# Kernel optimization log

Measured on AMD Instinct MI355X. Metric: run time of the kernel, lower is better.

The kernel has to match this reference:

```python
import jax, jax.numpy as jnp
import numpy as np

B, T, D_IN, D_H, D_OUT = 32, 2048, 1024, 1024, 1024

def setup_inputs() -> dict:
    key = jax.random.key(0)
    k1, k2, k3, k4, k5 = jax.random.split(key, 5)
    s = jax.random.normal(k1, (B, D_IN), dtype=jnp.float32)
    h = jax.random.normal(k2, (B, T, D_H), dtype=jnp.float32)
    # params (original uses np.random.random, i.e. uniform [0,1); scale kept modest)
    W_a = jax.random.uniform(k3, (D_IN, D_OUT), dtype=jnp.float32)
    U_a = jax.random.uniform(k4, (D_H, D_OUT), dtype=jnp.float32)
    v_a = jax.random.uniform(k5, (D_OUT,), dtype=jnp.float32)
    return {"s": s, "h": h, "W_a": W_a, "U_a": U_a, "v_a": v_a}

def reference(s, h, W_a, U_a, v_a):
    # Bahdanau additive attention:
    # e_bt = v_a . tanh(s W_a + h_t U_a);  a = softmax_t(e);  c_b = sum_t a_bt h_bt
    u_a_h = jnp.einsum('bth,ho->bto', h, U_a)            # [B,T,O]
    w_a_s = jnp.einsum('bi,io->bo', s, W_a)[:, None, :]  # [B,1,O]
    e = jnp.einsum('bto,o->bt', jnp.tanh(w_a_s + u_a_h), v_a)  # [B,T]
    a = jax.nn.softmax(e, axis=-1)                       # [B,T]
    c = jnp.einsum('bt,bth->bh', a, h)                   # [B,H]
    return c
```

## Files before the change

### kernel.cpp

```cpp
#include <hip/hip_runtime.h>
#include <hip/hip_bf16.h>
#include <stdint.h>

#define Bb 32
#define Tt 2048
#define Dd 1024

typedef float    f32x4 __attribute__((ext_vector_type(4)));
typedef _Float16 f16x8 __attribute__((ext_vector_type(8)));
typedef uint32_t u32;

#define WS_E     131072
#define WS_A     393216
#define WS_CP    655360
#define WS_UT    4849664

__device__ __forceinline__ void gll16(const void* g, const void* lds) {
  __builtin_amdgcn_global_load_lds(
      (const __attribute__((address_space(1))) u32*)(uintptr_t)g,
      (__attribute__((address_space(3))) u32*)(uint32_t)(uintptr_t)lds,
      16, 0, 0);
}

__global__ __launch_bounds__(256) void k_ws(const float* __restrict__ s,
                                            const float* __restrict__ W,
                                            float* __restrict__ w2_ws) {
  const int b = blockIdx.x >> 2;
  const int o = (blockIdx.x & 3) * 256 + threadIdx.x;
  __shared__ float s_sh[Dd];
#pragma unroll
  for (int j = 0; j < 4; ++j)
    s_sh[threadIdx.x + 256 * j] = s[b * Dd + threadIdx.x + 256 * j];
  __syncthreads();
  float acc = 0.f;
#pragma unroll 8
  for (int i = 0; i < Dd; ++i) acc += s_sh[i] * W[(size_t)i * Dd + o];
  w2_ws[b * Dd + o] = 2.f * acc;
}

__global__ __launch_bounds__(256) void k_ut(const float* __restrict__ U,
                                            uint8_t* __restrict__ U_ts) {
  const int i0 = (blockIdx.x >> 4) * 64;
  const int o0 = (blockIdx.x & 15) * 64;
  __shared__ float tile[64][65];
  const int tx = threadIdx.x & 63;
  const int ty = threadIdx.x >> 6;
#pragma unroll
  for (int jj = 0; jj < 16; ++jj)
    tile[tx][ty + 4 * jj] = U[(size_t)(i0 + ty + 4 * jj) * Dd + o0 + tx];
  __syncthreads();
#pragma unroll
  for (int it = 0; it < 2; ++it) {
    const int g = it * 256 + threadIdx.x;
    const int o_loc = g & 63;
    const int kg = g >> 6;
    const int o = o0 + o_loc;
    const int k = i0 + kg * 8;
    f16x8 r;
#pragma unroll
    for (int m = 0; m < 8; ++m) r[m] = (_Float16)tile[o_loc][kg * 8 + m];
    const int c    = (o >> 5) * 4 + (k >> 8);
    const int kk   = (k >> 5) & 7;
    const int half = (o >> 4) & 1;
    const int ln   = ((k >> 3) & 3) * 16 + (o & 15);
    *(f16x8*)(U_ts + (size_t)c * 16384 + kk * 2048 + half * 1024 + ln * 16) = r;
  }
}

__global__ __launch_bounds__(256, 2) void k_e(const float* __restrict__ h,
                                              const uint8_t* __restrict__ U_ts,
                                              const float* __restrict__ w2_ws,
                                              const float* __restrict__ v_a,
                                              float* __restrict__ e_ws) {
  const int b    = blockIdx.x >> 5;
  const int t0   = (blockIdx.x & 31) << 6;
  const int lane = threadIdx.x & 63;
  const int wv   = threadIdx.x >> 6;
  const int kh   = wv & 1;
  const int th   = wv >> 1;

  __shared__ __align__(16) uint8_t ubuf[2][16384];
  __shared__ __align__(16) float   exch[2048];

  f16x8 hreg[32];
  {
    const int tcol = t0 + th * 32 + (lane & 15);
    const int kgrp = (lane >> 4) * 8;
    const float* hb0 = h + ((size_t)b * Tt + tcol) * Dd;
    const float* hb1 = hb0 + (size_t)16 * Dd;
#pragma unroll
    for (int ss = 0; ss < 16; ++ss) {
      const int kbase = (ss >> 2) * 256 + kh * 128 + (ss & 3) * 32 + kgrp;
      f32x4 p0 = *(const f32x4*)(hb0 + kbase);
      f32x4 p1 = *(const f32x4*)(hb0 + kbase + 4);
      f16x8 r;
      r[0] = (_Float16)p0[0]; r[1] = (_Float16)p0[1];
      r[2] = (_Float16)p0[2]; r[3] = (_Float16)p0[3];
      r[4] = (_Float16)p1[0]; r[5] = (_Float16)p1[1];
      r[6] = (_Float16)p1[2]; r[7] = (_Float16)p1[3];
      hreg[ss * 2] = r;
      p0 = *(const f32x4*)(hb1 + kbase);
      p1 = *(const f32x4*)(hb1 + kbase + 4);
      r[0] = (_Float16)p0[0]; r[1] = (_Float16)p0[1];
      r[2] = (_Float16)p0[2]; r[3] = (_Float16)p0[3];
      r[4] = (_Float16)p1[0]; r[5] = (_Float16)p1[1];
      r[6] = (_Float16)p1[2]; r[7] = (_Float16)p1[3];
      hreg[ss * 2 + 1] = r;
    }
  }

  auto stage = [&](int c, int buf) {
    const uint8_t* src = U_ts + (size_t)c * 16384 + (size_t)(wv * 4) * 1024 + (size_t)lane * 16;
#pragma unroll
    for (int q = 0; q < 4; ++q)
      gll16(src + q * 1024, &ubuf[buf][(wv * 4 + q) * 1024]);
  };

  stage(0, 0);
  __syncthreads();

  float ep0 = 0.f, ep1 = 0.f;
  const float* wp  = w2_ws + b * Dd;
  const int    obl = kh * 16 + ((lane >> 4) << 2);

  for (int ot = 0; ot < 32; ++ot) {
    const f32x4 w4 = *(const f32x4*)(wp + (ot << 5) + obl);
    const f32x4 v4 = *(const f32x4*)(v_a + (ot << 5) + obl);
    f32x4 accA0 = {0.f,0.f,0.f,0.f}, accA1 = {0.f,0.f,0.f,0.f};
    f32x4 accB0 = {0.f,0.f,0.f,0.f}, accB1 = {0.f,0.f,0.f,0.f};
#pragma unroll
    for (int kc = 0; kc < 4; ++kc) {
      const int c   = ot * 4 + kc;
      const int cur = kc & 1;
      if (c + 1 < 128) stage(c + 1, cur ^ 1);
      const uint8_t* ub = &ubuf[cur][0] + kh * 8192 + lane * 16;
#pragma unroll
      for (int kkl = 0; kkl < 4; ++kkl) {
        const f16x8 a0 = *(const f16x8*)(ub + kkl * 2048);
        const f16x8 a1 = *(const f16x8*)(ub + kkl * 2048 + 1024);
        const f16x8 b0 = hreg[(kc * 4 + kkl) * 2];
        const f16x8 b1 = hreg[(kc * 4 + kkl) * 2 + 1];
        accA0 = __builtin_amdgcn_mfma_f32_16x16x32_f16(a0, b0, accA0, 0, 0, 0);
        accA1 = __builtin_amdgcn_mfma_f32_16x16x32_f16(a0, b1, accA1, 0, 0, 0);
        accB0 = __builtin_amdgcn_mfma_f32_16x16x32_f16(a1, b0, accB0, 0, 0, 0);
        accB1 = __builtin_amdgcn_mfma_f32_16x16x32_f16(a1, b1, accB1, 0, 0, 0);
      }
      __syncthreads();
    }
    {
      float* snd = exch + wv * 512 + lane * 4;
      if (kh == 0) { *(f32x4*)snd = accB0; *(f32x4*)(snd + 256) = accB1; }
      else         { *(f32x4*)snd = accA0; *(f32x4*)(snd + 256) = accA1; }
    }
    __syncthreads();
    {
      const float* rcv = exch + (wv ^ 1) * 512 + lane * 4;
      const f32x4 q0 = *(const f32x4*)rcv;
      const f32x4 q1 = *(const f32x4*)(rcv + 256);
      f32x4 x0, x1;
      if (kh == 0) { x0 = accA0 + q0; x1 = accA1 + q1; }
      else         { x0 = accB0 + q0; x1 = accB1 + q1; }
#pragma unroll
      for (int r = 0; r < 4; ++r) {
        const float e0 = __expf(__builtin_fmaf(x0[r], 2.f, w4[r]));
        const float e1 = __expf(__builtin_fmaf(x1[r], 2.f, w4[r]));
        ep0 += v4[r] * (1.f - 2.f / (e0 + 1.f));
        ep1 += v4[r] * (1.f - 2.f / (e1 + 1.f));
      }
    }
  }

  ep0 += __shfl_xor(ep0, 16, 64); ep0 += __shfl_xor(ep0, 32, 64);
  ep1 += __shfl_xor(ep1, 16, 64); ep1 += __shfl_xor(ep1, 32, 64);
  __syncthreads();
  if (kh == 1 && lane < 16) {
    exch[th * 32 + lane]      = ep0;
    exch[th * 32 + 16 + lane] = ep1;
  }
  __syncthreads();
  if (kh == 0 && lane < 16) {
    e_ws[b * Tt + t0 + th * 32 + lane]      = ep0 + exch[th * 32 + lane];
    e_ws[b * Tt + t0 + th * 32 + 16 + lane] = ep1 + exch[th * 32 + 16 + lane];
  }
}

__global__ __launch_bounds__(256) void k_sm(const float* __restrict__ e_ws,
                                            float* __restrict__ a_ws) {
  const int b = blockIdx.x;
  const int lane = threadIdx.x & 63;
  const int wv = threadIdx.x >> 6;
  __shared__ float red[8];
  float ev[8];
  float m = -1e30f;
#pragma unroll
  for (int j = 0; j < 8; ++j) {
    ev[j] = e_ws[b * Tt + threadIdx.x + 256 * j];
    m = fmaxf(m, ev[j]);
  }
#pragma unroll
  for (int sft = 1; sft < 64; sft <<= 1) m = fmaxf(m, __shfl_xor(m, sft, 64));
  if (lane == 0) red[wv] = m;
  __syncthreads();
  m = fmaxf(fmaxf(red[0], red[1]), fmaxf(red[2], red[3]));
  float sum = 0.f;
#pragma unroll
  for (int j = 0; j < 8; ++j) { ev[j] = __expf(ev[j] - m); sum += ev[j]; }
#pragma unroll
  for (int sft = 1; sft < 64; sft <<= 1) sum += __shfl_xor(sum, sft, 64);
  if (lane == 0) red[4 + wv] = sum;
  __syncthreads();
  const float inv = 1.f / (red[4] + red[5] + red[6] + red[7]);
#pragma unroll
  for (int j = 0; j < 8; ++j) a_ws[b * Tt + threadIdx.x + 256 * j] = ev[j] * inv;
}

__global__ __launch_bounds__(256) void k_c1(const float* __restrict__ h,
                                            const float* __restrict__ a_ws,
                                            float* __restrict__ cpart) {
  const int b  = blockIdx.x >> 5;
  const int tc = blockIdx.x & 31;
  const int t0 = tc << 6;
  __shared__ float a_sh[64];
  if (threadIdx.x < 64) a_sh[threadIdx.x] = a_ws[b * Tt + t0 + threadIdx.x];
  __syncthreads();
  f32x4 acc = {0.f, 0.f, 0.f, 0.f};
  const float* hb = h + ((size_t)b * Tt + t0) * Dd + threadIdx.x * 4;
#pragma unroll 4
  for (int t = 0; t < 64; ++t) {
    const f32x4 hv = *(const f32x4*)(hb + (size_t)t * Dd);
    acc += a_sh[t] * hv;
  }
  *(f32x4*)(cpart + ((size_t)(tc * 32 + b) << 10) + threadIdx.x * 4) = acc;
}

__global__ __launch_bounds__(256) void k_c2(const float* __restrict__ cpart,
                                            float* __restrict__ out) {
  const int gid = blockIdx.x * 256 + threadIdx.x;
  const int b = gid >> 10;
  const int d = gid & 1023;
  float sv = 0.f;
#pragma unroll
  for (int tc = 0; tc < 32; ++tc) sv += cpart[((size_t)(tc * 32 + b) << 10) + d];
  out[gid] = sv;
}

extern "C" void kernel_launch(void* const* d_in, const int* in_sizes, int n_in,
                              void* d_out, int out_size, void* d_ws, size_t ws_size,
                              hipStream_t stream) {
  (void)in_sizes; (void)n_in; (void)out_size; (void)ws_size;
  const float* s  = (const float*)d_in[0];
  const float* h  = (const float*)d_in[1];
  const float* W  = (const float*)d_in[2];
  const float* U  = (const float*)d_in[3];
  const float* v  = (const float*)d_in[4];
  uint8_t* ws = (uint8_t*)d_ws;
  float*   w2_ws = (float*)ws;
  float*   e_ws  = (float*)(ws + WS_E);
  float*   a_ws  = (float*)(ws + WS_A);
  float*   cpart = (float*)(ws + WS_CP);
  uint8_t* U_ts  = ws + WS_UT;

  k_ws<<<128, 256, 0, stream>>>(s, W, w2_ws);
  k_ut<<<256, 256, 0, stream>>>(U, U_ts);
  k_e <<<1024, 256, 0, stream>>>(h, U_ts, w2_ws, v, e_ws);
  k_sm<<<Bb, 256, 0, stream>>>(e_ws, a_ws);
  k_c1<<<1024, 256, 0, stream>>>(h, a_ws, cpart);
  k_c2<<<128, 256, 0, stream>>>(cpart, (float*)d_out);
}
```

Baseline: 306.8 us.

## Triple-buffer U tiles with one barrier per chunk and stage w/v in LDS

Moves the LDS staging of U chunks from double to triple buffering, prefetching two chunks ahead. Each chunk now uses a single raw s_barrier after a partial vmcnt wait instead of two __syncthreads. The w and v vectors are preloaded into shared memory so the global loads inside the epilogue are gone, and s_setprio raises priority around the MFMA block. The cost is more LDS per block, which may limit the intended two blocks per CU. Hand-written waitcnt and barrier placement risks races if the counts are wrong, and stage() now wraps around and issues redundant loads for the last chunks.

Measured after the change: 301.2 us. About the same (-1.8%).

```diff
diff --git a/kernel.cpp b/kernel.cpp
--- a/kernel.cpp
+++ b/kernel.cpp
@@ -79,8 +79,17 @@
   const int kh   = wv & 1;
   const int th   = wv >> 1;
 
-  __shared__ __align__(16) uint8_t ubuf[2][16384];
+  __shared__ __align__(16) uint8_t ubuf[3][16384];
   __shared__ __align__(16) float   exch[2048];
+  __shared__ float w_sh[Dd];
+  __shared__ float v_sh[Dd];
+
+#pragma unroll
+  for (int j = 0; j < 4; ++j) {
+    const int o = threadIdx.x + 256 * j;
+    w_sh[o] = w2_ws[b * Dd + o];
+    v_sh[o] = v_a[o];
+  }
 
   f16x8 hreg[32];
   {
@@ -109,6 +118,8 @@
     }
   }
 
+  asm volatile("s_waitcnt vmcnt(0) lgkmcnt(0)" ::: "memory");
+
   auto stage = [&](int c, int buf) {
     const uint8_t* src = U_ts + (size_t)c * 16384 + (size_t)(wv * 4) * 1024 + (size_t)lane * 16;
 #pragma unroll
@@ -117,23 +128,26 @@
   };
 
   stage(0, 0);
-  __syncthreads();
+  stage(1, 1);
 
   float ep0 = 0.f, ep1 = 0.f;
-  const float* wp  = w2_ws + b * Dd;
-  const int    obl = kh * 16 + ((lane >> 4) << 2);
+  const int obl = kh * 16 + ((lane >> 4) << 2);
+  int cur = 0;
 
   for (int ot = 0; ot < 32; ++ot) {
-    const f32x4 w4 = *(const f32x4*)(wp + (ot << 5) + obl);
-    const f32x4 v4 = *(const f32x4*)(v_a + (ot << 5) + obl);
     f32x4 accA0 = {0.f,0.f,0.f,0.f}, accA1 = {0.f,0.f,0.f,0.f};
     f32x4 accB0 = {0.f,0.f,0.f,0.f}, accB1 = {0.f,0.f,0.f,0.f};
 #pragma unroll
     for (int kc = 0; kc < 4; ++kc) {
-      const int c   = ot * 4 + kc;
-      const int cur = kc & 1;
-      if (c + 1 < 128) stage(c + 1, cur ^ 1);
+      const int c = ot * 4 + kc;
+      asm volatile("s_waitcnt vmcnt(4)" ::: "memory");
+      __builtin_amdgcn_sched_barrier(0);
+      __builtin_amdgcn_s_barrier();
+      __builtin_amdgcn_sched_barrier(0);
+      const int nxt = cur >= 1 ? cur - 1 : cur + 2;
+      stage((c + 2) & 127, nxt);
       const uint8_t* ub = &ubuf[cur][0] + kh * 8192 + lane * 16;
+      __builtin_amdgcn_s_setprio(1);
 #pragma unroll
       for (int kkl = 0; kkl < 4; ++kkl) {
         const f16x8 a0 = *(const f16x8*)(ub + kkl * 2048);
@@ -145,14 +159,18 @@
         accB0 = __builtin_amdgcn_mfma_f32_16x16x32_f16(a1, b0, accB0, 0, 0, 0);
         accB1 = __builtin_amdgcn_mfma_f32_16x16x32_f16(a1, b1, accB1, 0, 0, 0);
       }
-      __syncthreads();
+      __builtin_amdgcn_s_setprio(0);
+      cur = cur == 2 ? 0 : cur + 1;
     }
     {
       float* snd = exch + wv * 512 + lane * 4;
       if (kh == 0) { *(f32x4*)snd = accB0; *(f32x4*)(snd + 256) = accB1; }
       else         { *(f32x4*)snd = accA0; *(f32x4*)(snd + 256) = accA1; }
     }
-    __syncthreads();
+    asm volatile("s_waitcnt lgkmcnt(0)" ::: "memory");
+    __builtin_amdgcn_sched_barrier(0);
+    __builtin_amdgcn_s_barrier();
+    __builtin_amdgcn_sched_barrier(0);
     {
       const float* rcv = exch + (wv ^ 1) * 512 + lane * 4;
       const f32x4 q0 = *(const f32x4*)rcv;
@@ -160,12 +178,15 @@
       f32x4 x0, x1;
       if (kh == 0) { x0 = accA0 + q0; x1 = accA1 + q1; }
       else         { x0 = accB0 + q0; x1 = accB1 + q1; }
+      const int ob = (ot << 5) + obl;
 #pragma unroll
       for (int r = 0; r < 4; ++r) {
-        const float e0 = __expf(__builtin_fmaf(x0[r], 2.f, w4[r]));
-        const float e1 = __expf(__builtin_fmaf(x1[r], 2.f, w4[r]));
-        ep0 += v4[r] * (1.f - 2.f / (e0 + 1.f));
-        ep1 += v4[r] * (1.f - 2.f / (e1 + 1.f));
+        const float wr = w_sh[ob + r];
+        const float vr = v_sh[ob + r];
+        const float e0 = __expf(__builtin_fmaf(x0[r], 2.f, wr));
+        const float e1 = __expf(__builtin_fmaf(x1[r], 2.f, wr));
+        ep0 += vr * (1.f - 2.f / (e0 + 1.f));
+        ep1 += vr * (1.f - 2.f / (e1 + 1.f));
       }
     }
   }
```
